# Kernel tuning notes

Hardware: AMD Instinct MI355X
Metric: run time of the kernel (lower is better)

Reference implementation:

```python
import jax, jax.numpy as jnp
import numpy as np

B, T, P, C = 32, 16, 16, 2048
EPS = 1e-5


def setup_inputs() -> dict:
    key = jax.random.key(0)
    ks = jax.random.split(key, 9)
    s = 0.02
    return {
        "X": jax.random.normal(ks[0], (B, T, P, C), dtype=jnp.float32),
        "W_att": jax.random.normal(ks[1], (C, C), dtype=jnp.float32) * s,
        "b_att": jnp.zeros((C,), dtype=jnp.float32),
        "W1": jax.random.normal(ks[2], (C, C), dtype=jnp.float32) * s,
        "b1": jnp.zeros((C,), dtype=jnp.float32),
        "gamma": jnp.ones((C,), dtype=jnp.float32),
        "beta": jnp.zeros((C,), dtype=jnp.float32),
        "W2": jax.random.normal(ks[3], (C, C), dtype=jnp.float32) * s,
        "b2": jnp.zeros((C,), dtype=jnp.float32),
    }


def reference(X, W_att, b_att, W1, b1, gamma, beta, W2, b2):
    b, t, p, c = X.shape
    Xf = X.reshape(b * t, p, c)                                   # [BT, P, C]
    # per-frame attention gate: mean over parts -> Linear -> sigmoid
    attn = jax.nn.sigmoid(jnp.einsum("nc,dc->nd", Xf.mean(axis=1), W_att) + b_att)
    Xg = Xf * attn[:, None, :]                                    # gate each part
    # gcn: Linear -> per-frame BatchNorm1d (training stats over P) -> ReLU -> Linear
    h = jnp.einsum("npc,dc->npd", Xg, W1) + b1                    # [BT, P, C]
    mu = h.mean(axis=1, keepdims=True)
    var = jnp.mean(jnp.square(h - mu), axis=1, keepdims=True)     # biased var, as torch BN
    hn = (h - mu) * jax.lax.rsqrt(var + EPS) * gamma + beta
    out = jnp.einsum("npc,dc->npd", jax.nn.relu(hn), W2) + b2
    return out.reshape(b, t, p, c)
```

## Files before the change

kernel.cpp:

```cpp
#include <hip/hip_runtime.h>
#include <hip/hip_bf16.h>

typedef __attribute__((ext_vector_type(8))) short short8;
typedef __attribute__((ext_vector_type(4))) float f32x4;

static constexpr int Cdim = 2048;
static constexpr int NFRM = 512;
static constexpr int Pdim = 16;
static constexpr int MROWS = NFRM * Pdim;
static constexpr float EPS = 1e-5f;

__device__ __forceinline__ unsigned short f2b(float x) {
  union { float f; unsigned u; } v; v.f = x;
  unsigned r = v.u + 0x7fffu + ((v.u >> 16) & 1u);
  return (unsigned short)(r >> 16);
}

__device__ __forceinline__ void gload16(const void* g, void* l) {
  __builtin_amdgcn_global_load_lds(
      (const __attribute__((address_space(1))) unsigned int*)g,
      (__attribute__((address_space(3))) unsigned int*)l, 16, 0, 0);
}


__global__ __launch_bounds__(256) void cast3_kernel(
    const float* __restrict__ s0, const float* __restrict__ s1, const float* __restrict__ s2,
    unsigned short* __restrict__ d0, unsigned short* __restrict__ d1, unsigned short* __restrict__ d2)
{
  long i = (long)blockIdx.x * 256 + threadIdx.x;
  const float* s; unsigned short* d; long off;
  if (i < 1048576)      { s = s0; d = d0; off = i; }
  else if (i < 2097152) { s = s1; d = d1; off = i - 1048576; }
  else                  { s = s2; d = d2; off = i - 2097152; }
  float4 v = reinterpret_cast<const float4*>(s)[off];
  union { unsigned short u[4]; unsigned long long q; } o;
  o.u[0] = f2b(v.x); o.u[1] = f2b(v.y); o.u[2] = f2b(v.z); o.u[3] = f2b(v.w);
  *reinterpret_cast<unsigned long long*>(d + off * 4) = o.q;
}

__global__ __launch_bounds__(256) void mean_cast_kernel(
    const float* __restrict__ X, unsigned short* __restrict__ Mb)
{
  int idx = blockIdx.x * 256 + threadIdx.x;
  int n  = idx >> 9;
  int c4 = idx & 511;
  const float4* xp = reinterpret_cast<const float4*>(X) + (long)n * (Pdim * 512) + c4;
  float4 s = {0.f, 0.f, 0.f, 0.f};
  #pragma unroll
  for (int p = 0; p < Pdim; ++p) {
    float4 v = xp[(long)p * 512];
    s.x += v.x; s.y += v.y; s.z += v.z; s.w += v.w;
  }
  const float r = 1.f / 16.f;
  union { unsigned short u[4]; unsigned long long q; } o;
  o.u[0] = f2b(s.x * r); o.u[1] = f2b(s.y * r); o.u[2] = f2b(s.z * r); o.u[3] = f2b(s.w * r);
  *reinterpret_cast<unsigned long long*>(Mb + (long)idx * 4) = o.q;
}

__global__ __launch_bounds__(256) void gate_kernel(
    const float* __restrict__ X, const float* __restrict__ P0, const float* __restrict__ P1,
    const float* __restrict__ b_att, unsigned short* __restrict__ Xg)
{
  long idx = (long)blockIdx.x * 256 + threadIdx.x;
  int c4 = (int)(idx & 511);
  long np = idx >> 9;
  long n  = np >> 4;
  float4 x  = reinterpret_cast<const float4*>(X)[idx];
  float4 p0 = reinterpret_cast<const float4*>(P0)[n * 512 + c4];
  float4 p1 = reinterpret_cast<const float4*>(P1)[n * 512 + c4];
  float4 bb = reinterpret_cast<const float4*>(b_att)[c4];
  float4 a;
  a.x = 1.f / (1.f + __expf(-(p0.x + p1.x + bb.x)));
  a.y = 1.f / (1.f + __expf(-(p0.y + p1.y + bb.y)));
  a.z = 1.f / (1.f + __expf(-(p0.z + p1.z + bb.z)));
  a.w = 1.f / (1.f + __expf(-(p0.w + p1.w + bb.w)));
  union { unsigned short u[4]; unsigned long long q; } o;
  o.u[0] = f2b(x.x * a.x); o.u[1] = f2b(x.y * a.y);
  o.u[2] = f2b(x.z * a.z); o.u[3] = f2b(x.w * a.w);
  *reinterpret_cast<unsigned long long*>(Xg + idx * 4) = o.q;
}

__global__ __launch_bounds__(256) void gemm_att_sk(
    const unsigned short* __restrict__ A,
    const unsigned short* __restrict__ B,
    float* __restrict__ P)
{
  constexpr int N = 2048, K = 2048, KH = 1024;
  __shared__ unsigned short As[128 * 32];
  __shared__ unsigned short Bs[128 * 32];
  const int t = threadIdx.x;
  const int lane = t & 63;
  const int wid = t >> 6;
  const int wr = wid >> 1, wc = wid & 1;
  const int m0 = blockIdx.x * 128, n0 = blockIdx.y * 128;
  const int k0 = blockIdx.z * KH;
  float* out = P + (long)blockIdx.z * (512L * 2048);

  f32x4 acc[4][4];
  #pragma unroll
  for (int i = 0; i < 4; i++)
    #pragma unroll
    for (int j = 0; j < 4; j++) acc[i][j] = (f32x4){0.f, 0.f, 0.f, 0.f};

  const int srow = t >> 2;
  const int scol = (t & 3) * 8;
  const long aoff0 = (long)(m0 + srow) * K + scol;
  const long aoff1 = (long)(m0 + 64 + srow) * K + scol;
  const long boff0 = (long)(n0 + srow) * K + scol;
  const long boff1 = (long)(n0 + 64 + srow) * K + scol;
  char* AsB = (char*)As;
  char* BsB = (char*)Bs;

  const int fr = lane & 15;
  const int fk = (lane >> 4) * 8;

  for (int kt = k0; kt < k0 + KH; kt += 32) {
    __syncthreads();
    gload16(A + aoff0 + kt, AsB + t * 16);
    gload16(A + aoff1 + kt, AsB + 4096 + t * 16);
    gload16(B + boff0 + kt, BsB + t * 16);
    gload16(B + boff1 + kt, BsB + 4096 + t * 16);
    __syncthreads();
    short8 af[4], bfr[4];
    #pragma unroll
    for (int m = 0; m < 4; m++)
      af[m] = *reinterpret_cast<const short8*>(&As[(wr * 64 + m * 16 + fr) * 32 + fk]);
    #pragma unroll
    for (int n = 0; n < 4; n++)
      bfr[n] = *reinterpret_cast<const short8*>(&Bs[(wc * 64 + n * 16 + fr) * 32 + fk]);
    #pragma unroll
    for (int m = 0; m < 4; m++)
      #pragma unroll
      for (int n = 0; n < 4; n++)
        acc[m][n] = __builtin_amdgcn_mfma_f32_16x16x32_bf16(af[m], bfr[n], acc[m][n], 0, 0, 0);
  }

  const int l4 = lane >> 4;
  #pragma unroll
  for (int m = 0; m < 4; m++) {
    const int r0 = m0 + wr * 64 + m * 16 + l4 * 4;
    #pragma unroll
    for (int n = 0; n < 4; n++) {
      const int cn = n0 + wc * 64 + n * 16 + fr;
      #pragma unroll
      for (int j = 0; j < 4; j++)
        out[(long)(r0 + j) * N + cn] = acc[m][n][j];
    }
  }
}

template<int EPI>
__global__ __launch_bounds__(512, 2) void gemm256(
    const unsigned short* __restrict__ A,
    const unsigned short* __restrict__ Bp,
    int Kk, int Nn, int nbx,
    const float* __restrict__ bias,
    const float* __restrict__ gamma,
    const float* __restrict__ beta,
    float* __restrict__ Cf,
    unsigned short* __restrict__ Cb)
{
  __shared__ char lds[131072];
  const int t = threadIdx.x;
  const int lane = t & 63;
  const int wid = t >> 6;
  const int wr = wid >> 2;
  const int wc = wid & 3;

  const int nw = gridDim.x;
  const int wg = (blockIdx.x & 7) * (nw >> 3) + (blockIdx.x >> 3);
  const int bx = wg % nbx;
  const int by = wg / nbx;
  const int m0 = bx << 8, n0 = by << 8;

  const int NT = Kk >> 6;
  const int NI = NT >> 1;

  const long h64 = (long)64 * Kk, h128 = (long)128 * Kk;
  const int row0 = t >> 3;
  const int col0 = ((t & 7) * 8) ^ ((row0 & 7) << 3);
  const unsigned short* gA = A  + (long)(m0 + row0) * Kk + col0;
  const unsigned short* gB = Bp + (long)(n0 + row0) * Kk + col0;

  const int fr_ = lane & 15;
  const int cb0 = ((lane >> 4) << 4) ^ ((fr_ & 7) << 4);
  const int aB = (wr << 14) + fr_ * 128;
  const int bB = 32768 + ((wc >> 1) << 14) + ((wc & 1) << 13) + fr_ * 128;

#define STG(gp_, ko_, lo_) do { \
    const unsigned short* g0_ = (gp_) + (ko_); \
    gload16(g0_, lds + (lo_) + (t << 4)); \
    gload16(g0_ + h64, lds + (lo_) + 8192 + (t << 4)); } while (0)

#define LDSA(buf_, m_, ks_) (*(const short8*)(lds + (buf_) * 65536 + aB + (m_) * 2048 + (cb0 ^ ((ks_) << 6))))
#define LDSB(buf_, n_, ks_) (*(const short8*)(lds + (buf_) * 65536 + bB + (n_) * 2048 + (cb0 ^ ((ks_) << 6))))

#define RDAF(buf_, mb_) do { \
    af[0][0] = LDSA(buf_, (mb_) + 0, 0); af[0][1] = LDSA(buf_, (mb_) + 0, 1); \
    af[1][0] = LDSA(buf_, (mb_) + 1, 0); af[1][1] = LDSA(buf_, (mb_) + 1, 1); \
    af[2][0] = LDSA(buf_, (mb_) + 2, 0); af[2][1] = LDSA(buf_, (mb_) + 2, 1); \
    af[3][0] = LDSA(buf_, (mb_) + 3, 0); af[3][1] = LDSA(buf_, (mb_) + 3, 1); } while (0)

#define RDB(buf_, nb_, dst_) do { \
    dst_[0][0] = LDSB(buf_, (nb_) + 0, 0); dst_[0][1] = LDSB(buf_, (nb_) + 0, 1); \
    dst_[1][0] = LDSB(buf_, (nb_) + 1, 0); dst_[1][1] = LDSB(buf_, (nb_) + 1, 1); } while (0)

#define QUAD(mb_, nb_, b_) do { \
    _Pragma("unroll") \
    for (int mi = 0; mi < 4; ++mi) { \
      _Pragma("unroll") \
      for (int ni = 0; ni < 2; ++ni) { \
        acc[(mb_) + mi][(nb_) + ni] = __builtin_amdgcn_mfma_f32_16x16x32_bf16(af[mi][0], b_[ni][0], acc[(mb_) + mi][(nb_) + ni], 0, 0, 0); \
        acc[(mb_) + mi][(nb_) + ni] = __builtin_amdgcn_mfma_f32_16x16x32_bf16(af[mi][1], b_[ni][1], acc[(mb_) + mi][(nb_) + ni], 0, 0, 0); \
      } } } while (0)

#define MID() do { \
    __builtin_amdgcn_sched_barrier(0); \
    __builtin_amdgcn_s_barrier(); \
    asm volatile("s_waitcnt lgkmcnt(0)" ::: "memory"); \
    __builtin_amdgcn_sched_barrier(0); \
    __builtin_amdgcn_s_setprio(1); } while (0)
#define END() do { \
    __builtin_amdgcn_s_setprio(0); \
    __builtin_amdgcn_sched_barrier(0); \
    __builtin_amdgcn_s_barrier(); \
    __builtin_amdgcn_sched_barrier(0); } while (0)

#define VM4 asm volatile("s_waitcnt vmcnt(4)" ::: "memory")
#define VM6 asm volatile("s_waitcnt vmcnt(6)" ::: "memory")
#define VM0 asm volatile("s_waitcnt vmcnt(0)" ::: "memory")

  f32x4 acc[8][4];
  #pragma unroll
  for (int i = 0; i < 8; i++)
    #pragma unroll
    for (int j = 0; j < 4; j++) acc[i][j] = (f32x4){0.f, 0.f, 0.f, 0.f};

  short8 af[4][2], b23[2][2], b0E[2][2], b0O[2][2];

  STG(gA, 0, 0);
  STG(gA + h128, 0, 16384);
  STG(gB, 0, 32768);
  STG(gB + h128, 0, 49152);
  STG(gB, 64, 98304);
  STG(gB + h128, 64, 114688);
  VM4;
  __builtin_amdgcn_s_barrier();
  __builtin_amdgcn_sched_barrier(0);
  RDB(0, 0, b0E);

#define ITERBODY(LAST_) do { \
     \
    VM4; STG(gA, ko + 64, 65536); \
    RDAF(0, 0); \
    MID(); QUAD(0, 0, b0E); END(); \
     \
    STG(gA + h128, ko + 64, 81920); \
    RDB(0, 2, b23); \
    MID(); QUAD(0, 2, b23); END(); \
     \
    if (!(LAST_)) STG(gB, ko + 128, 32768); \
    RDAF(0, 4); \
    MID(); QUAD(4, 0, b0E); END(); \
     \
    if (LAST_) { VM4; } else { VM6; STG(gB + h128, ko + 128, 49152); } \
    RDB(1, 0, b0O); \
    MID(); QUAD(4, 2, b23); END(); \
     \
    if (LAST_) { VM0; } else { VM4; STG(gA, ko + 128, 0); } \
    RDAF(1, 0); \
    MID(); QUAD(0, 0, b0O); END(); \
     \
    if (!(LAST_)) STG(gA + h128, ko + 128, 16384); \
    RDB(1, 2, b23); \
    MID(); QUAD(0, 2, b23); END(); \
     \
    if (!(LAST_)) STG(gB, ko + 192, 98304); \
    RDAF(1, 4); \
    MID(); QUAD(4, 0, b0O); END(); \
     \
    if (!(LAST_)) { VM6; STG(gB + h128, ko + 192, 114688); RDB(0, 0, b0E); } \
    MID(); QUAD(4, 2, b23); END(); \
  } while (0)

  long ko = 0;
  for (int i = 0; i < NI - 1; ++i, ko += 128) {
    ITERBODY(0);
  }
  ITERBODY(1);

  const int l4 = lane >> 4;
  #pragma unroll
  for (int m = 0; m < 8; ++m) {
    const int r0 = m0 + wr * 128 + m * 16 + l4 * 4;
    #pragma unroll
    for (int n = 0; n < 4; ++n) {
      const int cn = n0 + wc * 64 + n * 16 + fr_;
      if constexpr (EPI == 1) {
        float s1 = 0.f, s2 = 0.f;
        #pragma unroll
        for (int j = 0; j < 4; j++) { float v = acc[m][n][j]; s1 += v; s2 += v * v; }
        s1 += __shfl_xor(s1, 16); s2 += __shfl_xor(s2, 16);
        s1 += __shfl_xor(s1, 32); s2 += __shfl_xor(s2, 32);
        const float mean = s1 * 0.0625f;
        const float var  = s2 * 0.0625f - mean * mean;
        const float sc = rsqrtf(var + EPS) * gamma[cn];
        const float sh = beta[cn] - mean * sc;
        #pragma unroll
        for (int j = 0; j < 4; j++) {
          float v = fmaxf(acc[m][n][j] * sc + sh, 0.f);
          Cb[(long)(r0 + j) * Nn + cn] = f2b(v);
        }
      } else {
        const float bb = bias[cn];
        #pragma unroll
        for (int j = 0; j < 4; j++)
          Cf[(long)(r0 + j) * Nn + cn] = acc[m][n][j] + bb;
      }
    }
  }
#undef STG
#undef LDSA
#undef LDSB
#undef RDAF
#undef RDB
#undef QUAD
#undef MID
#undef END
#undef VM4
#undef VM6
#undef VM0
#undef ITERBODY
}

extern "C" void kernel_launch(void* const* d_in, const int* in_sizes, int n_in,
                              void* d_out, int out_size, void* d_ws, size_t ws_size,
                              hipStream_t stream) {
  const float* X     = (const float*)d_in[0];
  const float* W_att = (const float*)d_in[1];
  const float* b_att = (const float*)d_in[2];
  const float* W1    = (const float*)d_in[3];
  const float* gamma = (const float*)d_in[5];
  const float* beta  = (const float*)d_in[6];
  const float* W2    = (const float*)d_in[7];
  const float* b2    = (const float*)d_in[8];
  float* out = (float*)d_out;

  char* ws = (char*)d_ws;
  unsigned short* Wab = (unsigned short*)(ws + 0);
  unsigned short* W1b = (unsigned short*)(ws + 8388608);
  unsigned short* W2b = (unsigned short*)(ws + 16777216);
  float*          Pat = (float*)        (ws + 25165824);
  unsigned short* Xg  = (unsigned short*)(ws + 33554432);
  unsigned short* Hr  = (unsigned short*)(ws + 67108864);
  unsigned short* Mb  = (unsigned short*)(ws + 67108864);

  hipLaunchKernelGGL(cast3_kernel, dim3(12288), dim3(256), 0, stream,
                     W_att, W1, W2, Wab, W1b, W2b);
  hipLaunchKernelGGL(mean_cast_kernel, dim3(1024), dim3(256), 0, stream, X, Mb);
  hipLaunchKernelGGL(gemm_att_sk, dim3(4, 16, 2), dim3(256), 0, stream,
                     Mb, Wab, Pat);
  hipLaunchKernelGGL(gate_kernel, dim3(16384), dim3(256), 0, stream,
                     X, Pat, Pat + 512L * 2048, b_att, Xg);
  hipLaunchKernelGGL((gemm256<1>), dim3(256), dim3(512), 0, stream,
                     Xg, W1b, Cdim, Cdim, 32, nullptr, gamma, beta, nullptr, Hr);
  hipLaunchKernelGGL((gemm256<2>), dim3(256), dim3(512), 0, stream,
                     Hr, W2b, Cdim, Cdim, 32, b2, nullptr, nullptr, out, nullptr);
}
```

Measured before the change: 192.9 us.

## Drop trailing barrier per MFMA phase and retune vmcnt waits in GEMM loop

The GEMM main loop used two workgroup barriers per compute phase (one before and one after each MFMA quad). This drops the trailing barrier so each phase has a single barrier, and moves and retunes the global-load vmcnt waits to match the new ordering of LDS buffer reuse. The aim is to cut barrier stalls and let waves drift more between phases. Without the trailing barrier there is a risk of LDS write-after-read races, where new global-to-LDS loads overwrite data other waves are still reading.

```diff
diff --git a/kernel.cpp b/kernel.cpp
--- a/kernel.cpp
+++ b/kernel.cpp
@@ -214,21 +214,15 @@
         acc[(mb_) + mi][(nb_) + ni] = __builtin_amdgcn_mfma_f32_16x16x32_bf16(af[mi][1], b_[ni][1], acc[(mb_) + mi][(nb_) + ni], 0, 0, 0); \
       } } } while (0)
 
-#define MID() do { \
+#define BARX() do { \
     __builtin_amdgcn_sched_barrier(0); \
     __builtin_amdgcn_s_barrier(); \
     asm volatile("s_waitcnt lgkmcnt(0)" ::: "memory"); \
-    __builtin_amdgcn_sched_barrier(0); \
-    __builtin_amdgcn_s_setprio(1); } while (0)
-#define END() do { \
-    __builtin_amdgcn_s_setprio(0); \
-    __builtin_amdgcn_sched_barrier(0); \
-    __builtin_amdgcn_s_barrier(); \
     __builtin_amdgcn_sched_barrier(0); } while (0)
 
-#define VM4 asm volatile("s_waitcnt vmcnt(4)" ::: "memory")
-#define VM6 asm volatile("s_waitcnt vmcnt(6)" ::: "memory")
-#define VM0 asm volatile("s_waitcnt vmcnt(0)" ::: "memory")
+#define PRIO1() __builtin_amdgcn_s_setprio(1)
+#define PRIO0() __builtin_amdgcn_s_setprio(0)
+#define VMC(n_) asm volatile("s_waitcnt vmcnt(" #n_ ")" ::: "memory")
 
   f32x4 acc[8][4];
   #pragma unroll
@@ -244,43 +238,44 @@
   STG(gB + h128, 0, 49152);
   STG(gB, 64, 98304);
   STG(gB + h128, 64, 114688);
-  VM4;
+  VMC(4);
   __builtin_amdgcn_s_barrier();
   __builtin_amdgcn_sched_barrier(0);
   RDB(0, 0, b0E);
 
 #define ITERBODY(LAST_) do { \
      \
-    VM4; STG(gA, ko + 64, 65536); \
+    STG(gA, ko + 64, 65536); \
     RDAF(0, 0); \
-    MID(); QUAD(0, 0, b0E); END(); \
+    BARX(); PRIO1(); QUAD(0, 0, b0E); PRIO0(); \
      \
     STG(gA + h128, ko + 64, 81920); \
     RDB(0, 2, b23); \
-    MID(); QUAD(0, 2, b23); END(); \
-     \
+    BARX(); PRIO1(); QUAD(0, 2, b23); PRIO0(); \
+     \
+    VMC(4); \
     if (!(LAST_)) STG(gB, ko + 128, 32768); \
     RDAF(0, 4); \
-    MID(); QUAD(4, 0, b0E); END(); \
-     \
-    if (LAST_) { VM4; } else { VM6; STG(gB + h128, ko + 128, 49152); } \
+    BARX(); PRIO1(); QUAD(4, 0, b0E); PRIO0(); \
+     \
+    if (LAST_) { VMC(0); } else { VMC(2); STG(gB + h128, ko + 128, 49152); } \
     RDB(1, 0, b0O); \
-    MID(); QUAD(4, 2, b23); END(); \
-     \
-    if (LAST_) { VM0; } else { VM4; STG(gA, ko + 128, 0); } \
+    BARX(); PRIO1(); QUAD(4, 2, b23); PRIO0(); \
+     \
+    if (!(LAST_)) STG(gA, ko + 128, 0); \
     RDAF(1, 0); \
-    MID(); QUAD(0, 0, b0O); END(); \
+    BARX(); PRIO1(); QUAD(0, 0, b0O); PRIO0(); \
      \
     if (!(LAST_)) STG(gA + h128, ko + 128, 16384); \
     RDB(1, 2, b23); \
-    MID(); QUAD(0, 2, b23); END(); \
-     \
-    if (!(LAST_)) STG(gB, ko + 192, 98304); \
+    BARX(); PRIO1(); QUAD(0, 2, b23); PRIO0(); \
+     \
+    if (!(LAST_)) { VMC(4); STG(gB, ko + 192, 98304); } \
     RDAF(1, 4); \
-    MID(); QUAD(4, 0, b0O); END(); \
-     \
-    if (!(LAST_)) { VM6; STG(gB + h128, ko + 192, 114688); RDB(0, 0, b0E); } \
-    MID(); QUAD(4, 2, b23); END(); \
+    BARX(); PRIO1(); QUAD(4, 0, b0O); PRIO0(); \
+     \
+    if (!(LAST_)) { VMC(2); STG(gB + h128, ko + 192, 114688); RDB(0, 0, b0E); } \
+    BARX(); PRIO1(); QUAD(4, 2, b23); PRIO0(); \
   } while (0)
 
   long ko = 0;
@@ -325,11 +320,10 @@
 #undef RDAF
 #undef RDB
 #undef QUAD
-#undef MID
-#undef END
-#undef VM4
-#undef VM6
-#undef VM0
+#undef BARX
+#undef PRIO1
+#undef PRIO0
+#undef VMC
 #undef ITERBODY
 }
 
```

New measurement: 188.4 us. 2.3% less time.
